# Performance work log

Hardware: AMD Instinct MI355X
Metric: run time of the kernel (lower is better)

The kernel has to match this reference:

```python
import jax, jax.numpy as jnp
import numpy as np

B, S, H = 8, 4096, 512

def setup_inputs() -> dict:
    key = jax.random.key(0)
    k1, k2 = jax.random.split(key)
    lstm_out = jax.random.normal(k1, (B, S, H), dtype=jnp.float32)
    W = jax.random.normal(k2, (2 * H, H), dtype=jnp.float32) * (1.0 / np.sqrt(H))
    b = jnp.zeros((2 * H,), dtype=jnp.float32)
    return {"lstm_out": lstm_out, "W": W, "b": b}

def reference(lstm_out, W, b):
    # noise_net: Linear(H, 2H) + Softplus
    noise = jax.nn.softplus(jnp.einsum('bsh,oh->bso', lstm_out, W) + b)  # [B,S,2H]
    Q = noise[:, :, :H]   # process noise
    R = noise[:, :, H:]   # observation noise

    def step(carry, inp):
        state, P = carry
        z, q, r = inp                      # each [B,H]
        P_pred = P + q
        K = P_pred / (P_pred + r + 1e-6)
        state = state + K * (z - state)
        P = (1.0 - K) * P_pred
        return (state, P), state

    state0 = lstm_out[:, 0, :]
    P0 = jnp.full_like(state0, 0.1)
    # time-major for scan: [S,B,H]
    xs = (jnp.swapaxes(lstm_out, 0, 1),
          jnp.swapaxes(Q, 0, 1),
          jnp.swapaxes(R, 0, 1))
    _, states = jax.lax.scan(step, (state0, P0), xs)  # [S,B,H]
    return jnp.swapaxes(states, 0, 1)  # [B,S,H]
```

## Files before the change

kernel.cpp:

```cpp
#include <hip/hip_runtime.h>
#include <hip/hip_bf16.h>

#define B_ 8
#define S_ 4096
#define H_ 512

using short8 = __attribute__((ext_vector_type(8))) short;
using f32x4  = __attribute__((ext_vector_type(4))) float;

__device__ __forceinline__ float bf2f(unsigned u16) {
    return __uint_as_float(u16 << 16);
}
__device__ __forceinline__ unsigned pk2bf(float x, float y) {
    __hip_bfloat162 h = __float22bfloat162_rn(make_float2(x, y));
    return *reinterpret_cast<unsigned*>(&h);
}
__device__ __forceinline__ float softplus_f(float x) {
    float sp = __logf(1.0f + __expf(x));
    return x > 15.0f ? x : sp;
}

typedef __attribute__((address_space(1))) void* gbl_ptr_t;
typedef __attribute__((address_space(3))) void* lds_ptr_t;
__device__ __forceinline__ void gload_lds16(const void* g, void* l) {
    __builtin_amdgcn_global_load_lds((gbl_ptr_t)g, (lds_ptr_t)l, 16, 0, 0);
}

#define BAR() do { asm volatile("" ::: "memory"); \
                   __builtin_amdgcn_s_barrier(); \
                   asm volatile("" ::: "memory"); } while (0)

#define WAIT_LGKM0() do { asm volatile("s_waitcnt lgkmcnt(0)" ::: "memory"); \
                          __builtin_amdgcn_sched_barrier(0); } while (0)

#define ASZ8 2097152u
#define TOT8 2162688u

__global__ __launch_bounds__(256)
void convert_bf16(const float* __restrict__ A, const float* __restrict__ Wm,
                  uint4* __restrict__ Ab, uint4* __restrict__ Wb) {
    for (unsigned i = blockIdx.x * 256u + threadIdx.x; i < TOT8; i += 2048u * 256u) {
        const float4* src; uint4* dst; unsigned off;
        if (i < ASZ8) { src = (const float4*)A;  dst = Ab; off = i; }
        else          { src = (const float4*)Wm; dst = Wb; off = i - ASZ8; }
        float4 a = src[2u * off], b = src[2u * off + 1u];
        uint4 o;
        o.x = pk2bf(a.x, a.y); o.y = pk2bf(a.z, a.w);
        o.z = pk2bf(b.x, b.y); o.w = pk2bf(b.z, b.w);
        dst[off] = o;
    }
}

#define TM 128
#define TN 128
#define BK 64

__global__ __launch_bounds__(256, 2)
void gemm_softplus(const unsigned short* __restrict__ Ab,
                   const unsigned short* __restrict__ Wb,
                   const float* __restrict__ bias,
                   unsigned* __restrict__ QR) {
    __shared__ unsigned short As[2][8192];
    __shared__ unsigned short Bs[2][8192];

    const int bid     = blockIdx.x;
    const int logical = (bid & 7) * 256 + (bid >> 3);
    const int bm = logical >> 3;
    const int bn = logical & 7;

    const int t    = threadIdx.x;
    const int wave = t >> 6;
    const int lane = t & 63;
    const int wm  = (wave >> 1) * 64;
    const int wn  = (wave & 1) * 64;
    const int l15 = lane & 15;
    const int l4  = lane >> 4;

    const int m0 = bm * TM;

    const int lr = lane >> 3;
    const int su = ((lane & 7) ^ lr) * 8;

    const unsigned short* agp[4];
    const unsigned short* bgp[4];
    int ldsoff[4];
#pragma unroll
    for (int i = 0; i < 4; ++i) {
        const int j   = wave * 4 + i;
        const int row = j * 8 + lr;
        agp[i] = Ab + (size_t)(m0 + row) * 512 + su;
        const int n = bn * 64 + (row & 31) + ((row & 64) >> 1) + ((row & 32) << 4);
        bgp[i] = Wb + (size_t)n * 512 + su;
        ldsoff[i] = j * 512;
    }

    f32x4 acc[4][4] = {};

#define STAGE(s) do { \
    const int _sl = (s) & 1; const int _kc = (s) * BK; \
    _Pragma("unroll") for (int i = 0; i < 4; ++i) { \
        gload_lds16(agp[i] + _kc, &As[_sl][ldsoff[i]]); \
        gload_lds16(bgp[i] + _kc, &Bs[_sl][ldsoff[i]]); \
    } \
} while (0)

#define COMPUTE(g, VMN) do { \
    const unsigned short* _a = &As[(g) & 1][0]; \
    const unsigned short* _b = &Bs[(g) & 1][0]; \
    asm volatile("s_waitcnt vmcnt(" #VMN ")" ::: "memory"); \
    BAR(); \
    _Pragma("unroll") for (int kk = 0; kk < 2; ++kk) { \
        short8 af[4], bf[4]; \
        _Pragma("unroll") for (int i = 0; i < 4; ++i) { \
            const int ra = wm + i * 16 + l15; \
            af[i] = *(const short8*)(_a + ra * 64 + (((kk * 4 + l4) ^ (ra & 7)) * 8)); \
            const int rb = wn + i * 16 + l15; \
            bf[i] = *(const short8*)(_b + rb * 64 + (((kk * 4 + l4) ^ (rb & 7)) * 8)); \
        } \
        WAIT_LGKM0(); \
        __builtin_amdgcn_s_setprio(1); \
        _Pragma("unroll") for (int i = 0; i < 4; ++i) \
        _Pragma("unroll") for (int j = 0; j < 4; ++j) \
            acc[i][j] = __builtin_amdgcn_mfma_f32_16x16x32_bf16(af[i], bf[j], acc[i][j], 0, 0, 0); \
        __builtin_amdgcn_s_setprio(0); \
    } \
    BAR(); \
} while (0)

    STAGE(0);
    for (int g = 0; g < 7; ++g) {
        STAGE(g + 1);
        COMPUTE(g, 8);
    }
    COMPUTE(7, 0);

#undef COMPUTE
#undef STAGE

#pragma unroll
    for (int j = 0; j < 2; ++j) {
        const int h  = bn * 64 + (wn >> 1) + j * 16 + l15;
        const float bq = bias[h];
        const float br = bias[h + 512];
#pragma unroll
        for (int i = 0; i < 4; ++i) {
            const int mb = m0 + wm + i * 16 + l4 * 4;
#pragma unroll
            for (int r = 0; r < 4; ++r) {
                const float qv = softplus_f(acc[i][j][r] + bq);
                const float rv = softplus_f(acc[i][j + 2][r] + br);
                QR[(size_t)(mb + r) * 512 + h] = pk2bf(qv, rv);
            }
        }
    }
}

#define CHUNK 128
#define WARM 64

__global__ __launch_bounds__(256, 2)
void kalman_scan(const float* __restrict__ z,
                 const unsigned* __restrict__ QR,
                 float* __restrict__ out) {
    const int t     = threadIdx.x;
    const int hb    = blockIdx.x & 1;
    const int b     = (blockIdx.x >> 1) & 7;
    const int chunk = blockIdx.x >> 4;
    const int h     = hb * 256 + t;
    const int s0    = chunk << 7;
    const int sw    = (chunk == 0) ? 0 : (s0 - WARM);
    const size_t base = ((size_t)(b * S_ + sw)) * 512 + h;

    const float*    zp  = z + base;
    const unsigned* qrp = (const unsigned*)QR + base;
    float*          op  = out + base;

    const int ng    = ((s0 + CHUNK) - sw) >> 3;
    const int skipg = (s0 - sw) >> 3;

    float    Z0[8], Z1[8], Z2[8], Z3[8], Z4[8], Z5[8], Z6[8], Z7[8];
    unsigned Q0[8], Q1[8], Q2[8], Q3[8], Q4[8], Q5[8], Q6[8], Q7[8];

#define LOADG(g, Zb, Qb) { const int _o = (g) * 8;                          \
    _Pragma("unroll") for (int u = 0; u < 8; ++u) {                         \
        Zb[u] = zp[(size_t)(_o + u) * 512]; Qb[u] = qrp[(size_t)(_o + u) * 512]; } }

#define COMP(g, Zb, Qb) { const int _o = (g) * 8; const bool _st = (g) >= skipg; \
    _Pragma("unroll") for (int u = 0; u < 8; ++u) {                         \
        const float q  = bf2f(Qb[u] & 0xffffu);                             \
        const float r  = bf2f(Qb[u] >> 16);                                 \
        const float Pp = P + q, rr = r + 1e-6f;                             \
        const float K  = Pp * __builtin_amdgcn_rcpf(Pp + rr);               \
        state = fmaf(K, Zb[u] - state, state); P = rr * K;                  \
        if (_st) op[(size_t)(_o + u) * 512] = state; } }

    LOADG(0, Z0, Q0); LOADG(1, Z1, Q1); LOADG(2, Z2, Q2); LOADG(3, Z3, Q3);

    float state = Z0[0];
    float P = 0.1f;

    for (int g = 0; g < ng; g += 8) {
        if (g + 4  < ng) LOADG(g + 4,  Z4, Q4); COMP(g,     Z0, Q0);
        if (g + 5  < ng) LOADG(g + 5,  Z5, Q5); COMP(g + 1, Z1, Q1);
        if (g + 6  < ng) LOADG(g + 6,  Z6, Q6); COMP(g + 2, Z2, Q2);
        if (g + 7  < ng) LOADG(g + 7,  Z7, Q7); COMP(g + 3, Z3, Q3);
        if (g + 8  < ng) LOADG(g + 8,  Z0, Q0); COMP(g + 4, Z4, Q4);
        if (g + 9  < ng) LOADG(g + 9,  Z1, Q1); COMP(g + 5, Z5, Q5);
        if (g + 10 < ng) LOADG(g + 10, Z2, Q2); COMP(g + 6, Z6, Q6);
        if (g + 11 < ng) LOADG(g + 11, Z3, Q3); COMP(g + 7, Z7, Q7);
    }
#undef LOADG
#undef COMP
}

extern "C" void kernel_launch(void* const* d_in, const int* in_sizes, int n_in,
                              void* d_out, int out_size, void* d_ws, size_t ws_size,
                              hipStream_t stream) {
    const float* lstm = (const float*)d_in[0];
    const float* Wm   = (const float*)d_in[1];
    const float* bias = (const float*)d_in[2];

    unsigned* QRw = (unsigned*)d_ws;

    unsigned short* Abf = (unsigned short*)d_out;
    unsigned short* Wbf = (unsigned short*)((char*)d_out + (32u << 20));

    hipLaunchKernelGGL(convert_bf16, dim3(2048), dim3(256), 0, stream,
                       lstm, Wm, (uint4*)Abf, (uint4*)Wbf);

    hipLaunchKernelGGL(gemm_softplus, dim3(2048), dim3(256), 0, stream,
                       Abf, Wbf, bias, QRw);

    hipLaunchKernelGGL(kalman_scan, dim3(512), dim3(256), 0, stream,
                       lstm, QRw, (float*)d_out);
}
```

Before: 201.2 us.

## Halve GEMM K-tile to raise occupancy with a new LDS swizzle

The bf16 GEMM now uses a K tile of 32 instead of 64, halving its LDS footprint and raising the launch-bounds occupancy hint from 2 to 5 blocks per CU. The global-to-LDS load mapping and XOR swizzle are redone for 32-wide rows, with precomputed read offsets. The main loop runs 16 slices of one MFMA k-step each instead of 8 slices of two. More resident blocks should hide memory latency better, at the cost of twice as many barriers per K and tighter register limits that could cause spills.

```diff
diff --git a/kernel.cpp b/kernel.cpp
--- a/kernel.cpp
+++ b/kernel.cpp
@@ -53,15 +53,15 @@
 
 #define TM 128
 #define TN 128
-#define BK 64
-
-__global__ __launch_bounds__(256, 2)
+#define BK 32
+
+__global__ __launch_bounds__(256, 5)
 void gemm_softplus(const unsigned short* __restrict__ Ab,
                    const unsigned short* __restrict__ Wb,
                    const float* __restrict__ bias,
                    unsigned* __restrict__ QR) {
-    __shared__ unsigned short As[2][8192];
-    __shared__ unsigned short Bs[2][8192];
+    __shared__ unsigned short As[2][4096];
+    __shared__ unsigned short Bs[2][4096];
 
     const int bid     = blockIdx.x;
     const int logical = (bid & 7) * 256 + (bid >> 3);
@@ -78,63 +78,60 @@
 
     const int m0 = bm * TM;
 
-    const int lr = lane >> 3;
-    const int su = ((lane & 7) ^ lr) * 8;
-
-    const unsigned short* agp[4];
-    const unsigned short* bgp[4];
-    int ldsoff[4];
-#pragma unroll
-    for (int i = 0; i < 4; ++i) {
-        const int j   = wave * 4 + i;
-        const int row = j * 8 + lr;
-        agp[i] = Ab + (size_t)(m0 + row) * 512 + su;
-        const int n = bn * 64 + (row & 31) + ((row & 64) >> 1) + ((row & 32) << 4);
-        bgp[i] = Wb + (size_t)n * 512 + su;
-        ldsoff[i] = j * 512;
-    }
+    const int lr2  = lane >> 2;
+    const int s_st = (lr2 + (lane >> 4)) & 3;
+    const int sg   = ((lane & 3) ^ s_st) * 8;
+    const int row0 = wave * 16 + lr2;
+    const int nr0 = bn * 64 + (row0 & 31) + ((row0 & 64) >> 1) + ((row0 & 32) << 4);
+    const unsigned short* ag0 = Ab + (size_t)(m0 + row0) * 512 + sg;
+    const unsigned short* bg0 = Wb + (size_t)nr0 * 512 + sg;
+    const unsigned short* ag1 = ag0 + (size_t)64 * 512;
+    const unsigned short* bg1 = bg0 + (size_t)32 * 512;
+    const int sd0 = wave * 512;
+    const int sd1 = sd0 + 2048;
+
+    const int s_rd = (l15 + (l15 >> 2)) & 3;
+    const int gsw  = (l4 ^ s_rd) * 8;
+    const int aoff = (wm + l15) * 32 + gsw;
+    const int boff = (wn + l15) * 32 + gsw;
 
     f32x4 acc[4][4] = {};
 
 #define STAGE(s) do { \
     const int _sl = (s) & 1; const int _kc = (s) * BK; \
-    _Pragma("unroll") for (int i = 0; i < 4; ++i) { \
-        gload_lds16(agp[i] + _kc, &As[_sl][ldsoff[i]]); \
-        gload_lds16(bgp[i] + _kc, &Bs[_sl][ldsoff[i]]); \
-    } \
+    gload_lds16(ag0 + _kc, &As[_sl][sd0]); \
+    gload_lds16(ag1 + _kc, &As[_sl][sd1]); \
+    gload_lds16(bg0 + _kc, &Bs[_sl][sd0]); \
+    gload_lds16(bg1 + _kc, &Bs[_sl][sd1]); \
 } while (0)
 
-#define COMPUTE(g, VMN) do { \
+#define SLICE(g, VMN, DOSTG) do { \
     const unsigned short* _a = &As[(g) & 1][0]; \
     const unsigned short* _b = &Bs[(g) & 1][0]; \
+    if (DOSTG) STAGE((g) + 1); \
     asm volatile("s_waitcnt vmcnt(" #VMN ")" ::: "memory"); \
     BAR(); \
-    _Pragma("unroll") for (int kk = 0; kk < 2; ++kk) { \
-        short8 af[4], bf[4]; \
-        _Pragma("unroll") for (int i = 0; i < 4; ++i) { \
-            const int ra = wm + i * 16 + l15; \
-            af[i] = *(const short8*)(_a + ra * 64 + (((kk * 4 + l4) ^ (ra & 7)) * 8)); \
-            const int rb = wn + i * 16 + l15; \
-            bf[i] = *(const short8*)(_b + rb * 64 + (((kk * 4 + l4) ^ (rb & 7)) * 8)); \
-        } \
-        WAIT_LGKM0(); \
-        __builtin_amdgcn_s_setprio(1); \
-        _Pragma("unroll") for (int i = 0; i < 4; ++i) \
-        _Pragma("unroll") for (int j = 0; j < 4; ++j) \
-            acc[i][j] = __builtin_amdgcn_mfma_f32_16x16x32_bf16(af[i], bf[j], acc[i][j], 0, 0, 0); \
-        __builtin_amdgcn_s_setprio(0); \
+    short8 af[4], bf[4]; \
+    _Pragma("unroll") for (int i = 0; i < 4; ++i) { \
+        af[i] = *(const short8*)(_a + aoff + i * 512); \
+        bf[i] = *(const short8*)(_b + boff + i * 512); \
     } \
+    WAIT_LGKM0(); \
+    __builtin_amdgcn_s_setprio(1); \
+    _Pragma("unroll") for (int i = 0; i < 4; ++i) \
+    _Pragma("unroll") for (int j = 0; j < 4; ++j) \
+        acc[i][j] = __builtin_amdgcn_mfma_f32_16x16x32_bf16(af[i], bf[j], acc[i][j], 0, 0, 0); \
+    __builtin_amdgcn_s_setprio(0); \
     BAR(); \
 } while (0)
 
     STAGE(0);
-    for (int g = 0; g < 7; ++g) {
-        STAGE(g + 1);
-        COMPUTE(g, 8);
-    }
-    COMPUTE(7, 0);
-
-#undef COMPUTE
+    for (int g = 0; g < 15; ++g) {
+        SLICE(g, 4, 1);
+    }
+    SLICE(15, 0, 0);
+
+#undef SLICE
 #undef STAGE
 
 #pragma unroll
```

Result: slower. 322.0 us (+60.1%).
